# Kernel tuning notes

Hardware: AMD Instinct MI355X
Metric: run time of the kernel (lower is better)

## Reference

```python
import jax, jax.numpy as jnp
import numpy as np

N_NODE = 2048   # nodes per graph
B = 32          # num_graphs
N = B * N_NODE  # batched node count
E = 1048576     # random edges (self loops added in reference)
C = 12          # in_channels = history window
H = 8           # attention heads
P = 9           # n_pred (out_channels)


def setup_inputs() -> dict:
    key = jax.random.key(0)
    ks = jax.random.split(key, 16)
    rn = lambda k, shp, s: jax.random.normal(k, shp, dtype=jnp.float32) * s
    return {
        "x": rn(ks[0], (N, C), 1.0),
        "edge_index": jax.random.randint(ks[1], (2, E), 0, N, dtype=jnp.int64),
        "W_gat": rn(ks[2], (C, H * C), 1.0 / np.sqrt(C)),
        "att_src": rn(ks[3], (H, C), 0.1),
        "att_dst": rn(ks[4], (H, C), 0.1),
        "bias_gat": rn(ks[5], (C,), 0.05),
        "Wih1": rn(ks[6], (4 * 32, N_NODE), 1.0 / np.sqrt(N_NODE)),
        "Whh1": rn(ks[7], (4 * 32, 32), 1.0 / np.sqrt(32)),
        "bih1": rn(ks[8], (4 * 32,), 0.05),
        "bhh1": rn(ks[9], (4 * 32,), 0.05),
        "Wih2": rn(ks[10], (4 * 128, 32), 1.0 / np.sqrt(32)),
        "Whh2": rn(ks[11], (4 * 128, 128), 1.0 / np.sqrt(128)),
        "bih2": rn(ks[12], (4 * 128,), 0.05),
        "bhh2": rn(ks[13], (4 * 128,), 0.05),
        "W_lin": rn(ks[14], (N_NODE * P, 128), 1.0 / np.sqrt(128)),
        "b_lin": rn(ks[15], (N_NODE * P,), 0.05),
    }


def _lstm(xs, Wih, Whh, bih, bhh):
    # xs: [T, B, in]; PyTorch gate order i, f, g, o
    Hh = Whh.shape[1]
    Bb = xs.shape[1]
    def step(carry, x):
        h, c = carry
        z = x @ Wih.T + h @ Whh.T + bih + bhh  # [B, 4H]
        i, f, g, o = jnp.split(z, 4, axis=-1)
        c = jax.nn.sigmoid(f) * c + jax.nn.sigmoid(i) * jnp.tanh(g)
        h = jax.nn.sigmoid(o) * jnp.tanh(c)
        return (h, c), h
    init = (jnp.zeros((Bb, Hh), xs.dtype), jnp.zeros((Bb, Hh), xs.dtype))
    _, ys = jax.lax.scan(step, init, xs)
    return ys


def reference(x, edge_index, W_gat, att_src, att_dst, bias_gat,
              Wih1, Whh1, bih1, bhh1, Wih2, Whh2, bih2, bhh2, W_lin, b_lin):
    # ---- GATConv (heads=8, concat=False, add_self_loops=True) ----
    loop = jnp.arange(N, dtype=edge_index.dtype)
    src = jnp.concatenate([edge_index[0], loop])  # message source j
    dst = jnp.concatenate([edge_index[1], loop])  # message target i
    h = (x @ W_gat).reshape(N, H, C)              # [N,H,C]
    a_s = jnp.einsum('nhc,hc->nh', h, att_src)
    a_d = jnp.einsum('nhc,hc->nh', h, att_dst)
    e = jax.nn.leaky_relu(a_s[src] + a_d[dst], 0.2)          # [E',H]
    e_max = jax.ops.segment_max(e, dst, num_segments=N)      # self loops ensure non-empty segments
    w = jnp.exp(e - e_max[dst])
    denom = jax.ops.segment_sum(w, dst, num_segments=N)
    alpha = w / denom[dst]                                   # [E',H]
    agg = jax.ops.segment_sum(alpha[:, :, None] * h[src], dst, num_segments=N)  # [N,H,C]
    g = agg.mean(axis=1) + bias_gat                          # concat=False -> head mean, [N,C]
    # (dropout is identity in eval mode)

    # ---- temporal stack ----
    seq = jnp.moveaxis(g.reshape(B, N_NODE, C), 2, 0)        # [T=C, B, N_NODE]
    h1 = _lstm(seq, Wih1, Whh1, bih1, bhh1)                  # [T,B,32]
    h2 = _lstm(h1, Wih2, Whh2, bih2, bhh2)                   # [T,B,128]
    y = h2[-1] @ W_lin.T + b_lin                             # [B, N_NODE*P]
    return y.reshape(B * N_NODE, P)
```

## Files before the change

kernel.cpp:

```cpp
#include <hip/hip_runtime.h>
#include <hip/hip_bf16.h>
#include <stdint.h>

#define NTOT 65536
#define NNODE 2048
#define CIN 12

__device__ __forceinline__ float bf2f(uint32_t u) {
    union { uint32_t i; float f; } v; v.i = u << 16; return v.f;
}
__device__ __forceinline__ uint16_t f2bf(float f) {
    union { float f; uint32_t i; } v; v.f = f;
    uint32_t x = v.i;
    uint32_t r = x + 0x7fffu + ((x >> 16) & 1u);
    return (uint16_t)(r >> 16);
}
__device__ __forceinline__ float bflo(uint32_t u) { return bf2f(u & 0xffffu); }
__device__ __forceinline__ float bfhi(uint32_t u) { return bf2f(u >> 16); }
__device__ __forceinline__ float sigmf(float x) { return 1.0f / (1.0f + __expf(-x)); }
__device__ __forceinline__ float lrelu(float v) { return v > 0.f ? v : 0.2f * v; }

#define O_WG   16
#define O_AS   1168
#define O_AD   1264
#define O_BIAS 1360
#define O_BIH1 1376
#define O_BHH1 1504
#define O_BIH2 1632
#define O_BHH2 2144
#define O_BLIN 2656
#define O_END  21088

__device__ __forceinline__ void cvt(const void* s, float* d, int i, int bf) {
    d[i] = bf ? bf2f(((const uint16_t*)s)[i]) : ((const float*)s)[i];
}

__global__ void __launch_bounds__(256) k_pre(
    const void* x, const int* __restrict__ e32,
    const void* wg, const void* as_, const void* ad_, const void* bs,
    const void* b1, const void* bb1, const void* b2, const void* bb2,
    const void* bl, float* __restrict__ ws, int* __restrict__ deg) {
    int tid = threadIdx.x, lane = tid & 63;
    uint32_t u = ((const uint16_t*)x)[2 * lane];
    uint32_t ex = (u >> 7) & 0xFF;
    bool sane = (ex >= 0x60 && ex <= 0x9F) || (u == 0);
    unsigned long long bsx = __ballot(sane);
    bool hi_zero = (e32[2 * lane + 1] == 0);
    unsigned long long bz = __ballot(hi_zero);
    int bf = (__popcll(bsx) >= 52) ? 1 : 0;
    int st = (__popcll(bz) == 64) ? 2 : 1;
    if (blockIdx.x == 0 && tid == 0) {
        ((int*)ws)[0] = bf; ((int*)ws)[1] = st; ((int*)ws)[2] = 0;
    }
    deg[blockIdx.x * 256 + tid] = 0;
    int i = blockIdx.x * 256 + tid;
    if (i < 1152)  { cvt(wg,  ws + O_WG,   i, bf); return; } i -= 1152;
    if (i < 96)    { cvt(as_, ws + O_AS,   i, bf); return; } i -= 96;
    if (i < 96)    { cvt(ad_, ws + O_AD,   i, bf); return; } i -= 96;
    if (i < 12)    { cvt(bs,  ws + O_BIAS, i, bf); return; } i -= 12;
    if (i < 128)   { cvt(b1,  ws + O_BIH1, i, bf); return; } i -= 128;
    if (i < 128)   { cvt(bb1, ws + O_BHH1, i, bf); return; } i -= 128;
    if (i < 512)   { cvt(b2,  ws + O_BIH2, i, bf); return; } i -= 512;
    if (i < 512)   { cvt(bb2, ws + O_BHH2, i, bf); return; } i -= 512;
    if (i < 18432) { cvt(bl,  ws + O_BLIN, i, bf); }
}

__global__ void __launch_bounds__(256) k_nfa(const void* __restrict__ xraw,
                                             const float* __restrict__ Wg,
                                             const float* __restrict__ att,
                                             const int* __restrict__ flags,
                                             const int* __restrict__ e, int E,
                                             int* __restrict__ deg, int* __restrict__ rank,
                                             float* __restrict__ a_s, float* __restrict__ a_d) {
    __shared__ float sx[384];
    __shared__ float sw[1152];
    __shared__ float satt[192];
    __shared__ float sh[3072];
    int tid = threadIdx.x;
    int n0 = blockIdx.x * 32;
    if (flags[0]) {
        const uint32_t* xp = (const uint32_t*)xraw;
        for (int i = tid; i < 192; i += 256) {
            uint32_t u = xp[n0 * 6 + i];
            sx[2 * i] = bflo(u); sx[2 * i + 1] = bfhi(u);
        }
    } else {
        const float* xp = (const float*)xraw;
        for (int i = tid; i < 384; i += 256) sx[i] = xp[n0 * 12 + i];
    }
    for (int i = tid; i < 1152; i += 256) sw[i] = Wg[i];
    if (tid < 192) satt[tid] = att[tid];
    {
        long st = flags[1];
        int chunk = (E + gridDim.x - 1) / gridDim.x;
        int ebase = blockIdx.x * chunk;
        int eend = min(ebase + chunk, E);
        for (int i = ebase + tid; i < eend; i += 256) {
            int d = e[st * (E + i)];
            rank[i] = atomicAdd(&deg[d], 1);
        }
    }
    __syncthreads();
#pragma unroll
    for (int r = 0; r < 12; r++) {
        int idx = r * 256 + tid;
        int n = idx / 96, o = idx % 96;
        float acc = 0.f;
#pragma unroll
        for (int k = 0; k < 12; k++) acc += sx[n * 12 + k] * sw[k * 96 + o];
        sh[idx] = acc;
    }
    __syncthreads();
    {
        int nl = tid >> 3, h = tid & 7;
        const float* hr = sh + nl * 96 + h * 12;
        float s = 0.f, dd = 0.f;
#pragma unroll
        for (int c = 0; c < 12; c++) {
            float v = hr[c];
            s += v * satt[h * 12 + c];
            dd += v * satt[96 + h * 12 + c];
        }
        a_s[n0 * 8 + tid] = s;
        a_d[n0 * 8 + tid] = dd;
    }
}

__global__ void k_scan(const int* __restrict__ deg, int* __restrict__ offs,
                       int* __restrict__ gcount) {
    __shared__ int s[256];
    __shared__ int base;
    int t = threadIdx.x, i = blockIdx.x * 256 + t;
    int v = deg[i];
    s[t] = v; __syncthreads();
    for (int off = 1; off < 256; off <<= 1) {
        int a = (t >= off) ? s[t - off] : 0;
        __syncthreads();
        s[t] += a;
        __syncthreads();
    }
    if (t == 255) base = atomicAdd(gcount, s[255]);
    __syncthreads();
    offs[i] = base + s[t] - v;
}

__global__ void k_scatter(const int* __restrict__ e, int E, const int* __restrict__ flags,
                          const int* __restrict__ offs, const int* __restrict__ rank,
                          int* __restrict__ ssrc) {
    int i = blockIdx.x * 256 + threadIdx.x;
    if (i < E) {
        long st = flags[1];
        int s = e[st * i];
        int d = e[st * (E + i)];
        ssrc[offs[d] + rank[i]] = s;
    }
}

__global__ void __launch_bounds__(256) k_agg(
    const void* __restrict__ xraw, const float* __restrict__ WgG,
    const float* __restrict__ a_s, const float* __restrict__ a_d,
    const int* __restrict__ offs, const int* __restrict__ deg,
    const int* __restrict__ ssrc, const float* __restrict__ bias,
    const int* __restrict__ flags, float* __restrict__ gT) {
    __shared__ float swg[1152];
    __shared__ float sres[4][12];
    int tid = threadIdx.x, wave = tid >> 6, lane = tid & 63;
    for (int i = tid; i < 1152; i += 256) swg[i] = WgG[i];
    __syncthreads();
    int node = blockIdx.x * 4 + wave;
    int beg = offs[node], d = deg[node];
    int sub = lane >> 3, h = lane & 7;
    float adh = a_d[node * 8 + h];
    int bf = flags[0];
    float acc[12];
    float wsum = 0.f;
#pragma unroll
    for (int c = 0; c < 12; c++) acc[c] = 0.f;
    if (sub == 0) {
        float w = __expf(lrelu(a_s[node * 8 + h] + adh));
        wsum = w;
        if (bf) {
            const uint2* xp = (const uint2*)((const uint16_t*)xraw + node * 12);
            uint2 u0 = xp[0], u1 = xp[1], u2 = xp[2];
            acc[0] = w * bflo(u0.x); acc[1] = w * bfhi(u0.x);
            acc[2] = w * bflo(u0.y); acc[3] = w * bfhi(u0.y);
            acc[4] = w * bflo(u1.x); acc[5] = w * bfhi(u1.x);
            acc[6] = w * bflo(u1.y); acc[7] = w * bfhi(u1.y);
            acc[8] = w * bflo(u2.x); acc[9] = w * bfhi(u2.x);
            acc[10] = w * bflo(u2.y); acc[11] = w * bfhi(u2.y);
        } else {
            const float4* xp = (const float4*)((const float*)xraw + node * 12);
            float4 v0 = xp[0], v1 = xp[1], v2 = xp[2];
            acc[0] = w * v0.x; acc[1] = w * v0.y; acc[2] = w * v0.z; acc[3] = w * v0.w;
            acc[4] = w * v1.x; acc[5] = w * v1.y; acc[6] = w * v1.z; acc[7] = w * v1.w;
            acc[8] = w * v2.x; acc[9] = w * v2.y; acc[10] = w * v2.z; acc[11] = w * v2.w;
        }
    }
    for (int base = 0; base < d; base += 8) {
        int k = base + sub;
        if (k < d) {
            int s = ssrc[beg + k];
            float w = __expf(lrelu(a_s[s * 8 + h] + adh));
            wsum += w;
            if (bf) {
                const uint2* xp = (const uint2*)((const uint16_t*)xraw + s * 12);
                uint2 u0 = xp[0], u1 = xp[1], u2 = xp[2];
                acc[0] += w * bflo(u0.x); acc[1] += w * bfhi(u0.x);
                acc[2] += w * bflo(u0.y); acc[3] += w * bfhi(u0.y);
                acc[4] += w * bflo(u1.x); acc[5] += w * bfhi(u1.x);
                acc[6] += w * bflo(u1.y); acc[7] += w * bfhi(u1.y);
                acc[8] += w * bflo(u2.x); acc[9] += w * bfhi(u2.x);
                acc[10] += w * bflo(u2.y); acc[11] += w * bfhi(u2.y);
            } else {
                const float4* xp = (const float4*)((const float*)xraw + s * 12);
                float4 v0 = xp[0], v1 = xp[1], v2 = xp[2];
                acc[0] += w * v0.x; acc[1] += w * v0.y; acc[2] += w * v0.z; acc[3] += w * v0.w;
                acc[4] += w * v1.x; acc[5] += w * v1.y; acc[6] += w * v1.z; acc[7] += w * v1.w;
                acc[8] += w * v2.x; acc[9] += w * v2.y; acc[10] += w * v2.z; acc[11] += w * v2.w;
            }
        }
    }
#pragma unroll
    for (int off = 8; off <= 32; off <<= 1) {
        wsum += __shfl_xor(wsum, off, 64);
#pragma unroll
        for (int c = 0; c < 12; c++) acc[c] += __shfl_xor(acc[c], off, 64);
    }
    float invw = 1.f / wsum;
#pragma unroll
    for (int c = 0; c < 12; c++) acc[c] *= invw;
    float p0 = 0.f, p1 = 0.f;
    const float* wcol = swg + h * 12;
#pragma unroll
    for (int k = 0; k < 12; k++) {
        float a = acc[k];
        p0 += a * wcol[k * 96 + sub];
        p1 += a * wcol[k * 96 + sub + 4];
    }
#pragma unroll
    for (int off = 1; off <= 4; off <<= 1) {
        p0 += __shfl_xor(p0, off, 64);
        p1 += __shfl_xor(p1, off, 64);
    }
    if (h == 0) {
        sres[wave][sub] = p0;
        if (sub >= 4) sres[wave][sub + 4] = p1;
    }
    __syncthreads();
    if (tid < 48) {
        int no = tid / 12, c = tid % 12;
        gT[c * NTOT + blockIdx.x * 4 + no] = sres[no][c] * 0.125f + bias[c];
    }
}

__global__ void __launch_bounds__(256) k_z1(const float* __restrict__ gT,
                                            const void* __restrict__ Wraw,
                                            const float* __restrict__ b1,
                                            const float* __restrict__ b2,
                                            const int* __restrict__ flags,
                                            float* __restrict__ Z1) {
    int t = blockIdx.x >> 3, bg = (blockIdx.x & 7) * 4;
    __shared__ float sv[4][2048];
    __shared__ float zp[2][4][128];
    int tid = threadIdx.x;
#pragma unroll
    for (int q = 0; q < 4; q++)
        for (int v = tid; v < 2048; v += 256) sv[q][v] = gT[t * NTOT + (bg + q) * NNODE + v];
    __syncthreads();
    int row = tid & 127, half = tid >> 7;
    float a0 = 0.f, a1 = 0.f, a2 = 0.f, a3 = 0.f;
    int hbase = half * 1024;
    if (flags[0]) {
        const uint4* wp = (const uint4*)((const uint16_t*)Wraw + row * 2048 + hbase);
        for (int k = 0; k < 128; k++) {
            uint4 u = wp[k];
            float w0 = bflo(u.x), w1 = bfhi(u.x), w2 = bflo(u.y), w3 = bfhi(u.y);
            float w4 = bflo(u.z), w5 = bfhi(u.z), w6 = bflo(u.w), w7 = bfhi(u.w);
#pragma unroll
            for (int q = 0; q < 4; q++) {
                float4 A = *(const float4*)&sv[q][hbase + 8 * k];
                float4 B = *(const float4*)&sv[q][hbase + 8 * k + 4];
                float r = w0 * A.x + w1 * A.y + w2 * A.z + w3 * A.w
                        + w4 * B.x + w5 * B.y + w6 * B.z + w7 * B.w;
                if (q == 0) a0 += r; else if (q == 1) a1 += r;
                else if (q == 2) a2 += r; else a3 += r;
            }
        }
    } else {
        const float4* wp = (const float4*)((const float*)Wraw + row * 2048 + hbase);
        for (int k = 0; k < 256; k++) {
            float4 w = wp[k];
#pragma unroll
            for (int q = 0; q < 4; q++) {
                float4 A = *(const float4*)&sv[q][hbase + 4 * k];
                float r = w.x * A.x + w.y * A.y + w.z * A.z + w.w * A.w;
                if (q == 0) a0 += r; else if (q == 1) a1 += r;
                else if (q == 2) a2 += r; else a3 += r;
            }
        }
    }
    zp[half][0][row] = a0; zp[half][1][row] = a1;
    zp[half][2][row] = a2; zp[half][3][row] = a3;
    __syncthreads();
    if (tid < 128) {
        float bb = b1[tid] + b2[tid];
#pragma unroll
        for (int q = 0; q < 4; q++)
            Z1[t * 4096 + (bg + q) * 128 + tid] = zp[0][q][tid] + zp[1][q][tid] + bb;
    }
}

__global__ void __launch_bounds__(512) k_tail(
    const float* __restrict__ Z1,
    const void* __restrict__ Whh1r,
    const void* __restrict__ Wih2r, const void* __restrict__ Whh2r,
    const float* __restrict__ b2i, const float* __restrict__ b2h,
    const int* __restrict__ flags, float* __restrict__ h2l) {
    int b = blockIdx.x, tid = threadIdx.x;
    __shared__ __align__(16) float h1s[12 * 32];
    __shared__ __align__(16) float hb1[32];
    __shared__ float zs2[12 * 512];
    __shared__ __align__(16) float hb[128];
    __shared__ float zb[512];
    int bf = flags[0];

    if (tid < 64) {
        int lane = tid;
        float wA[32], wB[32];
        if (bf) {
            const uint32_t* w1 = (const uint32_t*)Whh1r;
#pragma unroll
            for (int k = 0; k < 16; k++) {
                uint32_t u = w1[lane * 16 + k];
                wA[2 * k] = bflo(u); wA[2 * k + 1] = bfhi(u);
                uint32_t v = w1[(lane + 64) * 16 + k];
                wB[2 * k] = bflo(v); wB[2 * k + 1] = bfhi(v);
            }
        } else {
            const float* w1 = (const float*)Whh1r;
#pragma unroll
            for (int k = 0; k < 32; k++) {
                wA[k] = w1[lane * 32 + k];
                wB[k] = w1[(lane + 64) * 32 + k];
            }
        }
        float za[12], zg[12];
#pragma unroll
        for (int t = 0; t < 12; t++) {
            za[t] = Z1[t * 4096 + b * 128 + lane];
            zg[t] = Z1[t * 4096 + b * 128 + 64 + lane];
        }
        if (lane < 32) hb1[lane] = 0.f;
        __threadfence_block();
        float c = 0.f;
        for (int t = 0; t < 12; t++) {
            float d0 = za[t], d1 = zg[t];
#pragma unroll
            for (int k = 0; k < 8; k++) {
                float4 h4 = *(const float4*)&hb1[4 * k];
                d0 += wA[4*k]*h4.x + wA[4*k+1]*h4.y + wA[4*k+2]*h4.z + wA[4*k+3]*h4.w;
                d1 += wB[4*k]*h4.x + wB[4*k+1]*h4.y + wB[4*k+2]*h4.z + wB[4*k+3]*h4.w;
            }
            float e0 = __shfl_xor(d0, 32, 64);
            float e1 = __shfl_xor(d1, 32, 64);
            if (lane < 32) {
                c = sigmf(e0) * c + sigmf(d0) * tanhf(d1);
                float h = sigmf(e1) * tanhf(c);
                hb1[lane] = h;
                h1s[t * 32 + lane] = h;
            }
            __threadfence_block();
        }
    }
    __syncthreads();

    float zbias = b2i[tid] + b2h[tid];
    if (bf) {
        const uint4* wi = (const uint4*)((const uint16_t*)Wih2r + tid * 32);
        uint4 wa = wi[0], wb = wi[1], wc = wi[2], wd = wi[3];
#pragma unroll
        for (int t = 0; t < 12; t++) {
            const float4* hp = (const float4*)&h1s[t * 32];
            float4 h0 = hp[0], h1 = hp[1], h2 = hp[2], h3 = hp[3];
            float4 h4 = hp[4], h5 = hp[5], h6 = hp[6], h7 = hp[7];
            float z = zbias;
            z += bflo(wa.x)*h0.x + bfhi(wa.x)*h0.y + bflo(wa.y)*h0.z + bfhi(wa.y)*h0.w;
            z += bflo(wa.z)*h1.x + bfhi(wa.z)*h1.y + bflo(wa.w)*h1.z + bfhi(wa.w)*h1.w;
            z += bflo(wb.x)*h2.x + bfhi(wb.x)*h2.y + bflo(wb.y)*h2.z + bfhi(wb.y)*h2.w;
            z += bflo(wb.z)*h3.x + bfhi(wb.z)*h3.y + bflo(wb.w)*h3.z + bfhi(wb.w)*h3.w;
            z += bflo(wc.x)*h4.x + bfhi(wc.x)*h4.y + bflo(wc.y)*h4.z + bfhi(wc.y)*h4.w;
            z += bflo(wc.z)*h5.x + bfhi(wc.z)*h5.y + bflo(wc.w)*h5.z + bfhi(wc.w)*h5.w;
            z += bflo(wd.x)*h6.x + bfhi(wd.x)*h6.y + bflo(wd.y)*h6.z + bfhi(wd.y)*h6.w;
            z += bflo(wd.z)*h7.x + bfhi(wd.z)*h7.y + bflo(wd.w)*h7.z + bfhi(wd.w)*h7.w;
            zs2[t * 512 + tid] = z;
        }
    } else {
        const float4* wi = (const float4*)((const float*)Wih2r + tid * 32);
        float4 w0 = wi[0], w1 = wi[1], w2 = wi[2], w3 = wi[3];
        float4 w4 = wi[4], w5 = wi[5], w6 = wi[6], w7 = wi[7];
#pragma unroll
        for (int t = 0; t < 12; t++) {
            const float4* hp = (const float4*)&h1s[t * 32];
            float4 h0 = hp[0], h1 = hp[1], h2 = hp[2], h3 = hp[3];
            float4 h4 = hp[4], h5 = hp[5], h6 = hp[6], h7 = hp[7];
            float z = zbias;
            z += w0.x*h0.x + w0.y*h0.y + w0.z*h0.z + w0.w*h0.w;
            z += w1.x*h1.x + w1.y*h1.y + w1.z*h1.z + w1.w*h1.w;
            z += w2.x*h2.x + w2.y*h2.y + w2.z*h2.z + w2.w*h2.w;
            z += w3.x*h3.x + w3.y*h3.y + w3.z*h3.z + w3.w*h3.w;
            z += w4.x*h4.x + w4.y*h4.y + w4.z*h4.z + w4.w*h4.w;
            z += w5.x*h5.x + w5.y*h5.y + w5.z*h5.z + w5.w*h5.w;
            z += w6.x*h6.x + w6.y*h6.y + w6.z*h6.z + w6.w*h6.w;
            z += w7.x*h7.x + w7.y*h7.y + w7.z*h7.z + w7.w*h7.w;
            zs2[t * 512 + tid] = z;
        }
    }

    uint4 wreg[16];
    if (bf) {
        const uint4* p = (const uint4*)((const uint16_t*)Whh2r + tid * 128);
#pragma unroll
        for (int k = 0; k < 16; k++) wreg[k] = p[k];
    }
    const float4* wf = (const float4*)((const float*)Whh2r + tid * 128);
    if (tid < 128) hb[tid] = 0.f;
    float c2 = 0.f;
    __syncthreads();
    for (int t = 0; t < 12; t++) {
        float p0 = 0.f, p1 = 0.f, p2 = 0.f, p3 = 0.f;
        if (bf) {
#pragma unroll
            for (int k = 0; k < 8; k++) {
                float4 h0 = *(const float4*)&hb[16 * k];
                float4 h1 = *(const float4*)&hb[16 * k + 4];
                float4 h2 = *(const float4*)&hb[16 * k + 8];
                float4 h3 = *(const float4*)&hb[16 * k + 12];
                uint4 ua = wreg[2 * k], ub = wreg[2 * k + 1];
                p0 += bflo(ua.x)*h0.x + bfhi(ua.x)*h0.y + bflo(ua.y)*h0.z + bfhi(ua.y)*h0.w;
                p1 += bflo(ua.z)*h1.x + bfhi(ua.z)*h1.y + bflo(ua.w)*h1.z + bfhi(ua.w)*h1.w;
                p2 += bflo(ub.x)*h2.x + bfhi(ub.x)*h2.y + bflo(ub.y)*h2.z + bfhi(ub.y)*h2.w;
                p3 += bflo(ub.z)*h3.x + bfhi(ub.z)*h3.y + bflo(ub.w)*h3.z + bfhi(ub.w)*h3.w;
            }
        } else {
#pragma unroll
            for (int k = 0; k < 8; k++) {
                float4 h0 = *(const float4*)&hb[16 * k];
                float4 h1 = *(const float4*)&hb[16 * k + 4];
                float4 h2 = *(const float4*)&hb[16 * k + 8];
                float4 h3 = *(const float4*)&hb[16 * k + 12];
                float4 q0 = wf[4 * k], q1 = wf[4 * k + 1], q2 = wf[4 * k + 2], q3 = wf[4 * k + 3];
                p0 += q0.x*h0.x + q0.y*h0.y + q0.z*h0.z + q0.w*h0.w;
                p1 += q1.x*h1.x + q1.y*h1.y + q1.z*h1.z + q1.w*h1.w;
                p2 += q2.x*h2.x + q2.y*h2.y + q2.z*h2.z + q2.w*h2.w;
                p3 += q3.x*h3.x + q3.y*h3.y + q3.z*h3.z + q3.w*h3.w;
            }
        }
        zb[tid] = zs2[t * 512 + tid] + (p0 + p1) + (p2 + p3);
        __syncthreads();
        if (tid < 128) {
            float iv = zb[tid], fv = zb[128 + tid], gv = zb[256 + tid], ov = zb[384 + tid];
            c2 = sigmf(fv) * c2 + sigmf(iv) * tanhf(gv);
            float h = sigmf(ov) * tanhf(c2);
            hb[tid] = h;
            if (t == 11) h2l[b * 128 + tid] = h;
        }
        __syncthreads();
    }
}

__global__ void __launch_bounds__(256) k_lin(const float* __restrict__ h2l,
                                             const void* __restrict__ Wraw,
                                             const float* __restrict__ bl,
                                             const int* __restrict__ flags,
                                             void* __restrict__ outv) {
    __shared__ float hl[8 * 128];
    int bg = blockIdx.y;
    for (int i = threadIdx.x; i < 1024; i += 256) hl[i] = h2l[bg * 1024 + i];
    __syncthreads();
    int o = blockIdx.x * 256 + threadIdx.x;
    float bb = bl[o];
    float acc[8];
#pragma unroll
    for (int b = 0; b < 8; b++) acc[b] = bb;
    int bf = flags[0];
    if (bf) {
        const uint4* wp = (const uint4*)((const uint16_t*)Wraw + o * 128);
        for (int k = 0; k < 16; k++) {
            uint4 u = wp[k];
            float w0 = bflo(u.x), w1 = bfhi(u.x), w2 = bflo(u.y), w3 = bfhi(u.y);
            float w4 = bflo(u.z), w5 = bfhi(u.z), w6 = bflo(u.w), w7 = bfhi(u.w);
#pragma unroll
            for (int b = 0; b < 8; b++) {
                const float* h8 = hl + b * 128 + k * 8;
                acc[b] += w0 * h8[0] + w1 * h8[1] + w2 * h8[2] + w3 * h8[3]
                        + w4 * h8[4] + w5 * h8[5] + w6 * h8[6] + w7 * h8[7];
            }
        }
    } else {
        const float4* wp = (const float4*)((const float*)Wraw + o * 128);
        for (int k = 0; k < 32; k++) {
            float4 w = wp[k];
#pragma unroll
            for (int b = 0; b < 8; b++) {
                const float* h4 = hl + b * 128 + k * 4;
                acc[b] += w.x * h4[0] + w.y * h4[1] + w.z * h4[2] + w.w * h4[3];
            }
        }
    }
    if (bf) {
        uint16_t* out = (uint16_t*)outv;
#pragma unroll
        for (int b = 0; b < 8; b++) out[(bg * 8 + b) * 18432 + o] = f2bf(acc[b]);
    } else {
        float* out = (float*)outv;
#pragma unroll
        for (int b = 0; b < 8; b++) out[(bg * 8 + b) * 18432 + o] = acc[b];
    }
}

extern "C" void kernel_launch(void* const* d_in, const int* in_sizes, int n_in,
                              void* d_out, int out_size, void* d_ws, size_t ws_size,
                              hipStream_t stream) {
    int E = in_sizes[1] / 2;

    float* ws = (float*)d_ws;
    int* flags = (int*)ws;
    float* cWg   = ws + O_WG;
    float* cAtt  = ws + O_AS;
    float* cBias = ws + O_BIAS;
    float* cBih1 = ws + O_BIH1;
    float* cBhh1 = ws + O_BHH1;
    float* cBih2 = ws + O_BIH2;
    float* cBhh2 = ws + O_BHH2;
    float* cBlin = ws + O_BLIN;

    float* base = ws + O_END;
    float* a_s  = base;
    float* a_d  = a_s + 524288;
    int* deg    = (int*)(a_d + 524288);
    int* offs   = deg + 65536;
    int* rank   = offs + 65536;
    int* ssrc   = rank + E;
    float* gT   = (float*)(ssrc + E);
    float* Z1   = gT + 786432;
    float* h2l  = Z1 + 49152;
    size_t needed = (size_t)((h2l + 4096) - ws) * 4;
    if (ws_size < needed) return;

    k_pre<<<256, 256, 0, stream>>>(d_in[0], (const int*)d_in[1],
                                   d_in[2], d_in[3], d_in[4], d_in[5],
                                   d_in[8], d_in[9], d_in[12], d_in[13], d_in[15],
                                   ws, deg);
    k_nfa<<<2048, 256, 0, stream>>>(d_in[0], cWg, cAtt, flags,
                                    (const int*)d_in[1], E, deg, rank,
                                    a_s, a_d);
    k_scan<<<256, 256, 0, stream>>>(deg, offs, flags + 2);
    k_scatter<<<(E + 255) / 256, 256, 0, stream>>>((const int*)d_in[1], E, flags,
                                                   offs, rank, ssrc);
    k_agg<<<NTOT / 4, 256, 0, stream>>>(d_in[0], cWg, a_s, a_d, offs, deg, ssrc,
                                        cBias, flags, gT);
    k_z1<<<96, 256, 0, stream>>>(gT, d_in[6], cBih1, cBhh1, flags, Z1);
    k_tail<<<32, 512, 0, stream>>>(Z1, d_in[7], d_in[10], d_in[11],
                                   cBih2, cBhh2, flags, h2l);
    k_lin<<<dim3(72, 4), 256, 0, stream>>>(h2l, d_in[14], cBlin, flags, d_out);
}
```

Before: 381.8 us.

## Restructure LSTM tail to 256 threads with per-thread gate ownership and double-buffered h

Rewrites the second LSTM loop in k_tail so that each thread pair, split across half-waves, computes all four gates for one hidden unit and combines the two halves with a cross-lane shuffle. This removes the shared-memory gate buffer and one of the two block barriers per timestep. The hidden state is double-buffered, the input projection is kept in registers instead of shared memory, and sigmoid/tanh switch to fast reciprocal-based approximations. Block size drops from 512 to 256 threads, which raises per-thread register pressure (32 uint4 weight registers plus other arrays) and slightly changes numerics.

```diff
diff --git a/kernel.cpp b/kernel.cpp
--- a/kernel.cpp
+++ b/kernel.cpp
@@ -17,7 +17,13 @@
 }
 __device__ __forceinline__ float bflo(uint32_t u) { return bf2f(u & 0xffffu); }
 __device__ __forceinline__ float bfhi(uint32_t u) { return bf2f(u >> 16); }
-__device__ __forceinline__ float sigmf(float x) { return 1.0f / (1.0f + __expf(-x)); }
+__device__ __forceinline__ float sigmf(float x) {
+    return __builtin_amdgcn_rcpf(1.0f + __expf(-x));
+}
+__device__ __forceinline__ float tanhfast(float x) {
+    float ex = __expf(2.0f * x);
+    return 1.0f - 2.0f * __builtin_amdgcn_rcpf(ex + 1.0f);
+}
 __device__ __forceinline__ float lrelu(float v) { return v > 0.f ? v : 0.2f * v; }
 
 #define O_WG   16
@@ -310,7 +316,7 @@
     }
 }
 
-__global__ void __launch_bounds__(512) k_tail(
+__global__ void __launch_bounds__(256, 1) k_tail(
     const float* __restrict__ Z1,
     const void* __restrict__ Whh1r,
     const void* __restrict__ Wih2r, const void* __restrict__ Whh2r,
@@ -319,38 +325,76 @@
     int b = blockIdx.x, tid = threadIdx.x;
     __shared__ __align__(16) float h1s[12 * 32];
     __shared__ __align__(16) float hb1[32];
-    __shared__ float zs2[12 * 512];
-    __shared__ __align__(16) float hb[128];
-    __shared__ float zb[512];
+    __shared__ __align__(16) float hb[2][128];
     int bf = flags[0];
+    int lane = tid & 63, wv = tid >> 6;
+    int qh = lane >> 5;
+    int e = wv * 32 + (lane & 31);
+
+    int rA = e + 256 * qh;
+    int rB = e + 128 + 256 * qh;
+    float zbA = b2i[rA] + b2h[rA];
+    float zbB = b2i[rB] + b2h[rB];
+    float wA_[32], wB_[32];
+    uint4 wd[32];
+    if (bf) {
+        const uint16_t* W2 = (const uint16_t*)Whh2r;
+#pragma unroll
+        for (int q = 0; q < 4; q++) {
+            const uint4* p = (const uint4*)(W2 + (q * 128 + e) * 128 + qh * 64);
+#pragma unroll
+            for (int k = 0; k < 8; k++) wd[q * 8 + k] = p[k];
+        }
+        const uint4* wiA = (const uint4*)((const uint16_t*)Wih2r + rA * 32);
+        const uint4* wiB = (const uint4*)((const uint16_t*)Wih2r + rB * 32);
+#pragma unroll
+        for (int k = 0; k < 4; k++) {
+            uint4 ua = wiA[k], ub = wiB[k];
+            wA_[8 * k + 0] = bflo(ua.x); wA_[8 * k + 1] = bfhi(ua.x);
+            wA_[8 * k + 2] = bflo(ua.y); wA_[8 * k + 3] = bfhi(ua.y);
+            wA_[8 * k + 4] = bflo(ua.z); wA_[8 * k + 5] = bfhi(ua.z);
+            wA_[8 * k + 6] = bflo(ua.w); wA_[8 * k + 7] = bfhi(ua.w);
+            wB_[8 * k + 0] = bflo(ub.x); wB_[8 * k + 1] = bfhi(ub.x);
+            wB_[8 * k + 2] = bflo(ub.y); wB_[8 * k + 3] = bfhi(ub.y);
+            wB_[8 * k + 4] = bflo(ub.z); wB_[8 * k + 5] = bfhi(ub.z);
+            wB_[8 * k + 6] = bflo(ub.w); wB_[8 * k + 7] = bfhi(ub.w);
+        }
+    } else {
+        const float* Wi = (const float*)Wih2r;
+#pragma unroll
+        for (int k = 0; k < 32; k++) {
+            wA_[k] = Wi[rA * 32 + k];
+            wB_[k] = Wi[rB * 32 + k];
+        }
+    }
 
     if (tid < 64) {
-        int lane = tid;
+        int l = tid;
         float wA[32], wB[32];
         if (bf) {
             const uint32_t* w1 = (const uint32_t*)Whh1r;
 #pragma unroll
             for (int k = 0; k < 16; k++) {
-                uint32_t u = w1[lane * 16 + k];
+                uint32_t u = w1[l * 16 + k];
                 wA[2 * k] = bflo(u); wA[2 * k + 1] = bfhi(u);
-                uint32_t v = w1[(lane + 64) * 16 + k];
+                uint32_t v = w1[(l + 64) * 16 + k];
                 wB[2 * k] = bflo(v); wB[2 * k + 1] = bfhi(v);
             }
         } else {
             const float* w1 = (const float*)Whh1r;
 #pragma unroll
             for (int k = 0; k < 32; k++) {
-                wA[k] = w1[lane * 32 + k];
-                wB[k] = w1[(lane + 64) * 32 + k];
+                wA[k] = w1[l * 32 + k];
+                wB[k] = w1[(l + 64) * 32 + k];
             }
         }
         float za[12], zg[12];
 #pragma unroll
         for (int t = 0; t < 12; t++) {
-            za[t] = Z1[t * 4096 + b * 128 + lane];
-            zg[t] = Z1[t * 4096 + b * 128 + 64 + lane];
-        }
-        if (lane < 32) hb1[lane] = 0.f;
+            za[t] = Z1[t * 4096 + b * 128 + l];
+            zg[t] = Z1[t * 4096 + b * 128 + 64 + l];
+        }
+        if (l < 32) hb1[l] = 0.f;
         __threadfence_block();
         float c = 0.f;
         for (int t = 0; t < 12; t++) {
@@ -363,106 +407,79 @@
             }
             float e0 = __shfl_xor(d0, 32, 64);
             float e1 = __shfl_xor(d1, 32, 64);
-            if (lane < 32) {
-                c = sigmf(e0) * c + sigmf(d0) * tanhf(d1);
-                float h = sigmf(e1) * tanhf(c);
-                hb1[lane] = h;
-                h1s[t * 32 + lane] = h;
+            if (l < 32) {
+                c = sigmf(e0) * c + sigmf(d0) * tanhfast(d1);
+                float h = sigmf(e1) * tanhfast(c);
+                hb1[l] = h;
+                h1s[t * 32 + l] = h;
             }
             __threadfence_block();
         }
     }
-    __syncthreads();
-
-    float zbias = b2i[tid] + b2h[tid];
-    if (bf) {
-        const uint4* wi = (const uint4*)((const uint16_t*)Wih2r + tid * 32);
-        uint4 wa = wi[0], wb = wi[1], wc = wi[2], wd = wi[3];
-#pragma unroll
-        for (int t = 0; t < 12; t++) {
-            const float4* hp = (const float4*)&h1s[t * 32];
-            float4 h0 = hp[0], h1 = hp[1], h2 = hp[2], h3 = hp[3];
-            float4 h4 = hp[4], h5 = hp[5], h6 = hp[6], h7 = hp[7];
-            float z = zbias;
-            z += bflo(wa.x)*h0.x + bfhi(wa.x)*h0.y + bflo(wa.y)*h0.z + bfhi(wa.y)*h0.w;
-            z += bflo(wa.z)*h1.x + bfhi(wa.z)*h1.y + bflo(wa.w)*h1.z + bfhi(wa.w)*h1.w;
-            z += bflo(wb.x)*h2.x + bfhi(wb.x)*h2.y + bflo(wb.y)*h2.z + bfhi(wb.y)*h2.w;
-            z += bflo(wb.z)*h3.x + bfhi(wb.z)*h3.y + bflo(wb.w)*h3.z + bfhi(wb.w)*h3.w;
-            z += bflo(wc.x)*h4.x + bfhi(wc.x)*h4.y + bflo(wc.y)*h4.z + bfhi(wc.y)*h4.w;
-            z += bflo(wc.z)*h5.x + bfhi(wc.z)*h5.y + bflo(wc.w)*h5.z + bfhi(wc.w)*h5.w;
-            z += bflo(wd.x)*h6.x + bfhi(wd.x)*h6.y + bflo(wd.y)*h6.z + bfhi(wd.y)*h6.w;
-            z += bflo(wd.z)*h7.x + bfhi(wd.z)*h7.y + bflo(wd.w)*h7.z + bfhi(wd.w)*h7.w;
-            zs2[t * 512 + tid] = z;
-        }
-    } else {
-        const float4* wi = (const float4*)((const float*)Wih2r + tid * 32);
-        float4 w0 = wi[0], w1 = wi[1], w2 = wi[2], w3 = wi[3];
-        float4 w4 = wi[4], w5 = wi[5], w6 = wi[6], w7 = wi[7];
-#pragma unroll
-        for (int t = 0; t < 12; t++) {
-            const float4* hp = (const float4*)&h1s[t * 32];
-            float4 h0 = hp[0], h1 = hp[1], h2 = hp[2], h3 = hp[3];
-            float4 h4 = hp[4], h5 = hp[5], h6 = hp[6], h7 = hp[7];
-            float z = zbias;
-            z += w0.x*h0.x + w0.y*h0.y + w0.z*h0.z + w0.w*h0.w;
-            z += w1.x*h1.x + w1.y*h1.y + w1.z*h1.z + w1.w*h1.w;
-            z += w2.x*h2.x + w2.y*h2.y + w2.z*h2.z + w2.w*h2.w;
-            z += w3.x*h3.x + w3.y*h3.y + w3.z*h3.z + w3.w*h3.w;
-            z += w4.x*h4.x + w4.y*h4.y + w4.z*h4.z + w4.w*h4.w;
-            z += w5.x*h5.x + w5.y*h5.y + w5.z*h5.z + w5.w*h5.w;
-            z += w6.x*h6.x + w6.y*h6.y + w6.z*h6.z + w6.w*h6.w;
-            z += w7.x*h7.x + w7.y*h7.y + w7.z*h7.z + w7.w*h7.w;
-            zs2[t * 512 + tid] = z;
-        }
-    }
-
-    uint4 wreg[16];
-    if (bf) {
-        const uint4* p = (const uint4*)((const uint16_t*)Whh2r + tid * 128);
-#pragma unroll
-        for (int k = 0; k < 16; k++) wreg[k] = p[k];
-    }
-    const float4* wf = (const float4*)((const float*)Whh2r + tid * 128);
-    if (tid < 128) hb[tid] = 0.f;
+    if (tid < 128) hb[0][tid] = 0.f;
+    __syncthreads();
+
+    float zA[12], zB[12];
+#pragma unroll
+    for (int t = 0; t < 12; t++) {
+        const float4* hp = (const float4*)&h1s[t * 32];
+        float a = zbA, c = zbB;
+#pragma unroll
+        for (int k = 0; k < 8; k++) {
+            float4 h4 = hp[k];
+            a += wA_[4*k]*h4.x + wA_[4*k+1]*h4.y + wA_[4*k+2]*h4.z + wA_[4*k+3]*h4.w;
+            c += wB_[4*k]*h4.x + wB_[4*k+1]*h4.y + wB_[4*k+2]*h4.z + wB_[4*k+3]*h4.w;
+        }
+        zA[t] = a; zB[t] = c;
+    }
+
+    const float* W2f = (const float*)Whh2r;
+    const float4* wq0 = (const float4*)(W2f + (0 * 128 + e) * 128 + qh * 64);
+    const float4* wq1 = (const float4*)(W2f + (1 * 128 + e) * 128 + qh * 64);
+    const float4* wq2 = (const float4*)(W2f + (2 * 128 + e) * 128 + qh * 64);
+    const float4* wq3 = (const float4*)(W2f + (3 * 128 + e) * 128 + qh * 64);
     float c2 = 0.f;
-    __syncthreads();
+#pragma unroll
     for (int t = 0; t < 12; t++) {
-        float p0 = 0.f, p1 = 0.f, p2 = 0.f, p3 = 0.f;
+        const int cur = t & 1, nxt = cur ^ 1;
+        const float4* hp = (const float4*)&hb[cur][qh * 64];
+        float p0, p1, p2, p3;
+        if (qh == 0) { p0 = zA[t]; p1 = zB[t]; p2 = 0.f;   p3 = 0.f;   }
+        else         { p0 = 0.f;   p1 = 0.f;   p2 = zA[t]; p3 = zB[t]; }
         if (bf) {
 #pragma unroll
             for (int k = 0; k < 8; k++) {
-                float4 h0 = *(const float4*)&hb[16 * k];
-                float4 h1 = *(const float4*)&hb[16 * k + 4];
-                float4 h2 = *(const float4*)&hb[16 * k + 8];
-                float4 h3 = *(const float4*)&hb[16 * k + 12];
-                uint4 ua = wreg[2 * k], ub = wreg[2 * k + 1];
-                p0 += bflo(ua.x)*h0.x + bfhi(ua.x)*h0.y + bflo(ua.y)*h0.z + bfhi(ua.y)*h0.w;
-                p1 += bflo(ua.z)*h1.x + bfhi(ua.z)*h1.y + bflo(ua.w)*h1.z + bfhi(ua.w)*h1.w;
-                p2 += bflo(ub.x)*h2.x + bfhi(ub.x)*h2.y + bflo(ub.y)*h2.z + bfhi(ub.y)*h2.w;
-                p3 += bflo(ub.z)*h3.x + bfhi(ub.z)*h3.y + bflo(ub.w)*h3.z + bfhi(ub.w)*h3.w;
+                float4 ha = hp[2 * k], hc = hp[2 * k + 1];
+                uint4 u0 = wd[k], u1 = wd[8 + k], u2 = wd[16 + k], u3 = wd[24 + k];
+                p0 += bflo(u0.x)*ha.x + bfhi(u0.x)*ha.y + bflo(u0.y)*ha.z + bfhi(u0.y)*ha.w
+                    + bflo(u0.z)*hc.x + bfhi(u0.z)*hc.y + bflo(u0.w)*hc.z + bfhi(u0.w)*hc.w;
+                p1 += bflo(u1.x)*ha.x + bfhi(u1.x)*ha.y + bflo(u1.y)*ha.z + bfhi(u1.y)*ha.w
+                    + bflo(u1.z)*hc.x + bfhi(u1.z)*hc.y + bflo(u1.w)*hc.z + bfhi(u1.w)*hc.w;
+                p2 += bflo(u2.x)*ha.x + bfhi(u2.x)*ha.y + bflo(u2.y)*ha.z + bfhi(u2.y)*ha.w
+                    + bflo(u2.z)*hc.x + bfhi(u2.z)*hc.y + bflo(u2.w)*hc.z + bfhi(u2.w)*hc.w;
+                p3 += bflo(u3.x)*ha.x + bfhi(u3.x)*ha.y + bflo(u3.y)*ha.z + bfhi(u3.y)*ha.w
+                    + bflo(u3.z)*hc.x + bfhi(u3.z)*hc.y + bflo(u3.w)*hc.z + bfhi(u3.w)*hc.w;
             }
         } else {
 #pragma unroll
-            for (int k = 0; k < 8; k++) {
-                float4 h0 = *(const float4*)&hb[16 * k];
-                float4 h1 = *(const float4*)&hb[16 * k + 4];
-                float4 h2 = *(const float4*)&hb[16 * k + 8];
-                float4 h3 = *(const float4*)&hb[16 * k + 12];
-                float4 q0 = wf[4 * k], q1 = wf[4 * k + 1], q2 = wf[4 * k + 2], q3 = wf[4 * k + 3];
-                p0 += q0.x*h0.x + q0.y*h0.y + q0.z*h0.z + q0.w*h0.w;
-                p1 += q1.x*h1.x + q1.y*h1.y + q1.z*h1.z + q1.w*h1.w;
-                p2 += q2.x*h2.x + q2.y*h2.y + q2.z*h2.z + q2.w*h2.w;
-                p3 += q3.x*h3.x + q3.y*h3.y + q3.z*h3.z + q3.w*h3.w;
-            }
-        }
-        zb[tid] = zs2[t * 512 + tid] + (p0 + p1) + (p2 + p3);
-        __syncthreads();
-        if (tid < 128) {
-            float iv = zb[tid], fv = zb[128 + tid], gv = zb[256 + tid], ov = zb[384 + tid];
-            c2 = sigmf(fv) * c2 + sigmf(iv) * tanhf(gv);
-            float h = sigmf(ov) * tanhf(c2);
-            hb[tid] = h;
-            if (t == 11) h2l[b * 128 + tid] = h;
+            for (int k = 0; k < 16; k++) {
+                float4 h4 = hp[k];
+                float4 a0 = wq0[k], a1 = wq1[k], a2 = wq2[k], a3 = wq3[k];
+                p0 += a0.x*h4.x + a0.y*h4.y + a0.z*h4.z + a0.w*h4.w;
+                p1 += a1.x*h4.x + a1.y*h4.y + a1.z*h4.z + a1.w*h4.w;
+                p2 += a2.x*h4.x + a2.y*h4.y + a2.z*h4.z + a2.w*h4.w;
+                p3 += a3.x*h4.x + a3.y*h4.y + a3.z*h4.z + a3.w*h4.w;
+            }
+        }
+        float z0 = p0 + __shfl_xor(p0, 32, 64);
+        float z1 = p1 + __shfl_xor(p1, 32, 64);
+        float z2 = p2 + __shfl_xor(p2, 32, 64);
+        float z3 = p3 + __shfl_xor(p3, 32, 64);
+        c2 = sigmf(z1) * c2 + sigmf(z0) * tanhfast(z2);
+        float h = sigmf(z3) * tanhfast(c2);
+        if (qh == 0) {
+            hb[nxt][e] = h;
+            if (t == 11) h2l[b * 128 + e] = h;
         }
         __syncthreads();
     }
@@ -560,7 +577,7 @@
     k_agg<<<NTOT / 4, 256, 0, stream>>>(d_in[0], cWg, a_s, a_d, offs, deg, ssrc,
                                         cBias, flags, gT);
     k_z1<<<96, 256, 0, stream>>>(gT, d_in[6], cBih1, cBhh1, flags, Z1);
-    k_tail<<<32, 512, 0, stream>>>(Z1, d_in[7], d_in[10], d_in[11],
+    k_tail<<<32, 256, 0, stream>>>(Z1, d_in[7], d_in[10], d_in[11],
                                    cBih2, cBhh2, flags, h2l);
     k_lin<<<dim3(72, 4), 256, 0, stream>>>(h2l, d_in[14], cBlin, flags, d_out);
 }
```

Result: slower. 449.7 us (+17.8%).
